# Optimization experiments

Hardware: AMD Instinct MI355X
Metric: run time of the kernel (lower is better)

Reference implementation:

```python
import jax, jax.numpy as jnp
import numpy as np

N_HEADS = 16
MAX_LEN = 1024


def setup_inputs() -> dict:
    key = jax.random.key(0)
    ks = jax.random.split(key, 6)
    B, T, C = 4, 1024, 1024
    scale = 0.02
    return {
        "x": jax.random.normal(ks[0], (B, T, C), dtype=jnp.float32),
        "qkv_w": jax.random.normal(ks[1], (3 * C, C), dtype=jnp.float32) * scale,
        "qkv_b": jax.random.normal(ks[2], (3 * C,), dtype=jnp.float32) * scale,
        "proj_w": jax.random.normal(ks[3], (C, C), dtype=jnp.float32) * scale,
        "proj_b": jax.random.normal(ks[4], (C,), dtype=jnp.float32) * scale,
        "rel_pos_emb": jax.random.normal(ks[5], (2 * MAX_LEN - 1, C), dtype=jnp.float32) * scale,
    }


def reference(x, qkv_w, qkv_b, proj_w, proj_b, rel_pos_emb):
    B, T, C = x.shape
    H = N_HEADS
    D = C // H
    # QKV projection: (B,T,3C) -> (3,B,H,T,D)
    qkv = (x @ qkv_w.T + qkv_b).reshape(B, T, 3, H, D)
    qkv = jnp.transpose(qkv, (2, 0, 3, 1, 4))
    q, k, v = qkv[0], qkv[1], qkv[2]
    # scores: (B,H,T,T)
    att = jnp.einsum("bhtd,bhsd->bhts", q, k) / np.sqrt(D).astype(np.float32)
    # Relative position bias: gather-then-sum == sum-then-gather over head_dim.
    # Pre-reduce table to (2*max_len-1, H) to avoid materializing (T,T,C).
    table = rel_pos_emb.reshape(2 * MAX_LEN - 1, H, D).sum(axis=-1)  # (2L-1, H)
    pos = jnp.arange(T)
    rel_idx = pos[:, None] - pos[None, :] + (MAX_LEN - 1)  # (T,T)
    bias = jnp.transpose(table[rel_idx], (2, 0, 1))  # (H,T,T)
    att = att + bias[None]
    # causal mask: positions j > i masked to -inf
    causal = pos[None, :] > pos[:, None]  # (T,T) True above diagonal
    att = jnp.where(causal[None, None], -jnp.inf, att)
    att = jax.nn.softmax(att, axis=-1)
    out = jnp.einsum("bhts,bhsd->bhtd", att, v)  # (B,H,T,D)
    out = jnp.transpose(out, (0, 2, 1, 3)).reshape(B, T, C)
    return out @ proj_w.T + proj_b
```

## Files before the change

### kernel.cpp

```cpp
#include <hip/hip_runtime.h>
#include <hip/hip_bf16.h>


typedef __bf16 bf16x8 __attribute__((ext_vector_type(8)));
typedef float f32x4 __attribute__((ext_vector_type(4)));

__device__ __forceinline__ float bf2f(unsigned short u) {
    return __uint_as_float(((unsigned)u) << 16);
}
__device__ __forceinline__ unsigned short f2bf(float f) {
    __hip_bfloat16 h = __float2bfloat16(f);
    return *reinterpret_cast<unsigned short*>(&h);
}
__device__ __forceinline__ int4 cvt8(float4 a, float4 b) {
    union { unsigned short s[8]; int4 v; } u;
    u.s[0] = f2bf(a.x); u.s[1] = f2bf(a.y); u.s[2] = f2bf(a.z); u.s[3] = f2bf(a.w);
    u.s[4] = f2bf(b.x); u.s[5] = f2bf(b.y); u.s[6] = f2bf(b.z); u.s[7] = f2bf(b.w);
    return u.v;
}

__global__ __launch_bounds__(256) void table_reduce(const float* __restrict__ rel,
                                                    float* __restrict__ table) {
    const int p = blockIdx.x;
    const int tid = threadIdx.x, lane = tid & 63, wave = tid >> 6;
    const float* r = rel + (size_t)p * 1024;
    float s[4];
#pragma unroll
    for (int k = 0; k < 4; ++k) s[k] = r[tid + 256 * k];
#pragma unroll
    for (int k = 0; k < 4; ++k) {
        float v = s[k];
        for (int o = 32; o; o >>= 1) v += __shfl_xor(v, o, 64);
        if (lane == 0) table[p * 16 + wave + 4 * k] = v;
    }
}

template <int EPI, bool AF32>
__global__ __launch_bounds__(512) void gemm_bt(const void* __restrict__ Ain,
                                               const float* __restrict__ Bf,
                                               const float* __restrict__ bias,
                                               unsigned short* __restrict__ outb,
                                               float* __restrict__ outf,
                                               int M, int N, int K) {
    __shared__ __attribute__((aligned(16))) unsigned short As[128 * 40];
    __shared__ __attribute__((aligned(16))) unsigned short Bs[128 * 40];
    const int bm = blockIdx.x * 128, bn = blockIdx.y * 128;
    const int tid = threadIdx.x, lane = tid & 63, wave = tid >> 6;
    const int wr = wave & 1, wc = wave >> 1;
    const int quad = lane >> 4, lm = lane & 15;

    const int srow = tid >> 2;
    const int scol = (tid & 3) * 8;
    const float* ApF          = (const float*)Ain + (size_t)(bm + srow) * K + scol;
    const unsigned short* ApH = (const unsigned short*)Ain + (size_t)(bm + srow) * K + scol;
    const float* BpF          = Bf + (size_t)(bn + srow) * K + scol;
    unsigned short* AsW = &As[srow * 40 + scol];
    unsigned short* BsW = &Bs[srow * 40 + scol];

    f32x4 acc[4][2];
#pragma unroll
    for (int r = 0; r < 4; ++r)
#pragma unroll
        for (int c = 0; c < 2; ++c) acc[r][c] = (f32x4){0.f, 0.f, 0.f, 0.f};

    float4 paf0, paf1, pbf0, pbf1;
    int4 pah;
    if (AF32) {
        paf0 = *(const float4*)(ApF);
        paf1 = *(const float4*)(ApF + 4);
    } else {
        pah = *(const int4*)(ApH);
    }
    pbf0 = *(const float4*)(BpF);
    pbf1 = *(const float4*)(BpF + 4);

    for (int kk = 0; kk < K; kk += 32) {
        *(int4*)(AsW) = AF32 ? cvt8(paf0, paf1) : pah;
        *(int4*)(BsW) = cvt8(pbf0, pbf1);
        __syncthreads();

        if (kk + 32 < K) {
            if (AF32) {
                paf0 = *(const float4*)(ApF + kk + 32);
                paf1 = *(const float4*)(ApF + kk + 36);
            } else {
                pah = *(const int4*)(ApH + kk + 32);
            }
            pbf0 = *(const float4*)(BpF + kk + 32);
            pbf1 = *(const float4*)(BpF + kk + 36);
        }

        bf16x8 af[4], bfr[2];
#pragma unroll
        for (int r = 0; r < 4; ++r)
            af[r] = *(const bf16x8*)(&As[(64 * wr + 16 * r + lm) * 40 + quad * 8]);
#pragma unroll
        for (int c = 0; c < 2; ++c)
            bfr[c] = *(const bf16x8*)(&Bs[(32 * wc + 16 * c + lm) * 40 + quad * 8]);
#pragma unroll
        for (int r = 0; r < 4; ++r)
#pragma unroll
            for (int c = 0; c < 2; ++c)
                acc[r][c] = __builtin_amdgcn_mfma_f32_16x16x32_bf16(af[r], bfr[c], acc[r][c], 0, 0, 0);
        __syncthreads();
    }

#pragma unroll
    for (int r = 0; r < 4; ++r)
#pragma unroll
        for (int c = 0; c < 2; ++c)
#pragma unroll
            for (int i = 0; i < 4; ++i) {
                const int row = bm + 64 * wr + 16 * r + quad * 4 + i;
                const int col = bn + 32 * wc + 16 * c + lm;
                const float v = acc[r][c][i] + bias[col];
                if (EPI == 0) {
                    const int b = row >> 10, t = row & 1023;
                    const int s3 = col >> 10, rem = col & 1023;
                    const int h = rem >> 6, d = rem & 63;
                    const size_t base = (((size_t)s3 * 4 + b) * 16 + h) * 65536;
                    const size_t off = base + (s3 == 2 ? (size_t)d * 1024 + t
                                                       : (size_t)t * 64 + d);
                    outb[off] = f2bf(v);
                } else {
                    outf[(size_t)row * N + col] = v;
                }
            }
}

__global__ __launch_bounds__(512) void attn_mfma(const unsigned short* __restrict__ qkvb,
                                                 const float* __restrict__ table,
                                                 unsigned short* __restrict__ y) {
    const int bh = blockIdx.x, b = bh >> 4, h = bh & 15;
    const int qb = (7 - blockIdx.y) * 128;
    const int tid = threadIdx.x, lane = tid & 63, wave = tid >> 6;
    const int quad = lane >> 4, lm = lane & 15;

    __shared__ __attribute__((aligned(16))) unsigned short Ks[64][72];
    __shared__ __attribute__((aligned(16))) unsigned short Vs[64][72];
    __shared__ __attribute__((aligned(16))) unsigned short Ps[8][16][72];
    __shared__ float tb[1280];

    const unsigned short* Qg  = qkvb + ((size_t)(b)*16 + h) * 65536;
    const unsigned short* Kg  = qkvb + ((size_t)(4 + b)*16 + h) * 65536;
    const unsigned short* Vtg = qkvb + ((size_t)(8 + b)*16 + h) * 65536;

    const bf16x8 qf0 = *(const bf16x8*)(Qg + (size_t)(qb + wave * 16 + lm) * 64 + quad * 8);
    const bf16x8 qf1 = *(const bf16x8*)(Qg + (size_t)(qb + wave * 16 + lm) * 64 + 32 + quad * 8);

    const int tbn = qb + 255;
    for (int i = tid; i < tbn; i += 512) tb[i] = table[(896 + i) * 16 + h];

    f32x4 oacc[4];
#pragma unroll
    for (int nb = 0; nb < 4; ++nb) oacc[nb] = (f32x4){0.f, 0.f, 0.f, 0.f};
    float mi[4], li[4];
#pragma unroll
    for (int i = 0; i < 4; ++i) { mi[i] = -1e30f; li[i] = 0.f; }

    const int ktiles = qb / 64 + 2;
    for (int kt = 0; kt < ktiles; ++kt) {
        __syncthreads();
        {
            const int r0 = tid >> 3, c0 = (tid & 7) * 8;
            *(int4*)&Ks[r0][c0] = *(const int4*)(Kg + (size_t)(kt * 64 + r0) * 64 + c0);
            *(int4*)&Vs[r0][c0] = *(const int4*)(Vtg + (size_t)r0 * 1024 + kt * 64 + c0);
        }
        __syncthreads();

        f32x4 s[4];
#pragma unroll
        for (int nb = 0; nb < 4; ++nb) {
            bf16x8 k0 = *(const bf16x8*)(&Ks[nb * 16 + lm][quad * 8]);
            bf16x8 k1 = *(const bf16x8*)(&Ks[nb * 16 + lm][32 + quad * 8]);
            s[nb] = (f32x4){0.f, 0.f, 0.f, 0.f};
            s[nb] = __builtin_amdgcn_mfma_f32_16x16x32_bf16(qf0, k0, s[nb], 0, 0, 0);
            s[nb] = __builtin_amdgcn_mfma_f32_16x16x32_bf16(qf1, k1, s[nb], 0, 0, 0);
        }

        const int qrow0 = qb + wave * 16 + quad * 4;
        const int jbase = kt * 64 + lm;
#pragma unroll
        for (int nb = 0; nb < 4; ++nb)
#pragma unroll
            for (int i = 0; i < 4; ++i) {
                const int q = qrow0 + i, j = jbase + nb * 16;
                const float v = fmaf(s[nb][i], 0.125f, tb[q - j + 127]);
                s[nb][i] = (j <= q) ? v : -1e30f;
            }

        float mnew[4], al[4];
#pragma unroll
        for (int i = 0; i < 4; ++i) {
            float mx = fmaxf(fmaxf(s[0][i], s[1][i]), fmaxf(s[2][i], s[3][i]));
            mx = fmaxf(mx, __shfl_xor(mx, 1, 64));
            mx = fmaxf(mx, __shfl_xor(mx, 2, 64));
            mx = fmaxf(mx, __shfl_xor(mx, 4, 64));
            mx = fmaxf(mx, __shfl_xor(mx, 8, 64));
            mnew[i] = fmaxf(mi[i], mx);
            al[i] = __expf(mi[i] - mnew[i]);
            mi[i] = mnew[i];
        }
#pragma unroll
        for (int nb = 0; nb < 4; ++nb)
#pragma unroll
            for (int i = 0; i < 4; ++i) s[nb][i] = __expf(s[nb][i] - mnew[i]);
#pragma unroll
        for (int i = 0; i < 4; ++i) {
            float sm = (s[0][i] + s[1][i]) + (s[2][i] + s[3][i]);
            sm += __shfl_xor(sm, 1, 64);
            sm += __shfl_xor(sm, 2, 64);
            sm += __shfl_xor(sm, 4, 64);
            sm += __shfl_xor(sm, 8, 64);
            li[i] = li[i] * al[i] + sm;
        }

#pragma unroll
        for (int nb = 0; nb < 4; ++nb)
#pragma unroll
            for (int i = 0; i < 4; ++i)
                Ps[wave][quad * 4 + i][nb * 16 + lm] = f2bf(s[nb][i]);

#pragma unroll
        for (int nb = 0; nb < 4; ++nb)
#pragma unroll
            for (int i = 0; i < 4; ++i) oacc[nb][i] *= al[i];

        const bf16x8 p0 = *(const bf16x8*)(&Ps[wave][lm][quad * 8]);
        const bf16x8 p1 = *(const bf16x8*)(&Ps[wave][lm][32 + quad * 8]);
#pragma unroll
        for (int nb = 0; nb < 4; ++nb) {
            bf16x8 v0 = *(const bf16x8*)(&Vs[nb * 16 + lm][quad * 8]);
            bf16x8 v1 = *(const bf16x8*)(&Vs[nb * 16 + lm][32 + quad * 8]);
            oacc[nb] = __builtin_amdgcn_mfma_f32_16x16x32_bf16(p0, v0, oacc[nb], 0, 0, 0);
            oacc[nb] = __builtin_amdgcn_mfma_f32_16x16x32_bf16(p1, v1, oacc[nb], 0, 0, 0);
        }
    }

    float inv[4];
#pragma unroll
    for (int i = 0; i < 4; ++i) inv[i] = 1.0f / li[i];
#pragma unroll
    for (int nb = 0; nb < 4; ++nb)
#pragma unroll
        for (int i = 0; i < 4; ++i) {
            const int q = qb + wave * 16 + quad * 4 + i;
            const int d = nb * 16 + lm;
            y[((size_t)(b * 1024 + q)) * 1024 + h * 64 + d] = f2bf(oacc[nb][i] * inv[i]);
        }
}

extern "C" void kernel_launch(void* const* d_in, const int* in_sizes, int n_in,
                              void* d_out, int out_size, void* d_ws, size_t ws_size,
                              hipStream_t stream) {
    const float* x      = (const float*)d_in[0];
    const float* qkv_w  = (const float*)d_in[1];
    const float* qkv_b  = (const float*)d_in[2];
    const float* proj_w = (const float*)d_in[3];
    const float* proj_b = (const float*)d_in[4];
    const float* rel    = (const float*)d_in[5];
    float* out = (float*)d_out;

    char* ws = (char*)d_ws;
    float* table         = (float*)(ws + 16777216);
    unsigned short* qkvb = (unsigned short*)(ws + 16908288);
    unsigned short* yb   = (unsigned short*)(ws + 42074112);

    table_reduce<<<2047, 256, 0, stream>>>(rel, table);
    gemm_bt<0, true><<<dim3(32, 24), 512, 0, stream>>>(x, qkv_w, qkv_b, qkvb, nullptr,
                                                       4096, 3072, 1024);
    attn_mfma<<<dim3(64, 8), 512, 0, stream>>>(qkvb, table, yb);
    gemm_bt<1, false><<<dim3(32, 8), 512, 0, stream>>>(yb, proj_w, proj_b, nullptr, out,
                                                       4096, 1024, 1024);
}
```

Baseline: 205.6 us.

## Deepen GEMM K-tile to 64 and prefetch K/V tiles in attention loop

The GEMM kernel now stages 64-wide K slices in shared memory (padded row stride 72) and runs two MFMA sub-steps per barrier pair, which halves the number of loop iterations and synchronizations. The attention kernel now register-prefetches the next K/V tile while computing on the current one, so global loads overlap with compute, with the trailing barrier moved to the end of the loop. This costs more registers and shared memory per block, which may lower occupancy.

```diff
diff --git a/kernel.cpp b/kernel.cpp
--- a/kernel.cpp
+++ b/kernel.cpp
@@ -42,20 +42,20 @@
                                                unsigned short* __restrict__ outb,
                                                float* __restrict__ outf,
                                                int M, int N, int K) {
-    __shared__ __attribute__((aligned(16))) unsigned short As[128 * 40];
-    __shared__ __attribute__((aligned(16))) unsigned short Bs[128 * 40];
+    __shared__ __attribute__((aligned(16))) unsigned short As[128 * 72];
+    __shared__ __attribute__((aligned(16))) unsigned short Bs[128 * 72];
     const int bm = blockIdx.x * 128, bn = blockIdx.y * 128;
     const int tid = threadIdx.x, lane = tid & 63, wave = tid >> 6;
     const int wr = wave & 1, wc = wave >> 1;
     const int quad = lane >> 4, lm = lane & 15;
 
     const int srow = tid >> 2;
-    const int scol = (tid & 3) * 8;
+    const int scol = (tid & 3) * 16;
     const float* ApF          = (const float*)Ain + (size_t)(bm + srow) * K + scol;
     const unsigned short* ApH = (const unsigned short*)Ain + (size_t)(bm + srow) * K + scol;
     const float* BpF          = Bf + (size_t)(bn + srow) * K + scol;
-    unsigned short* AsW = &As[srow * 40 + scol];
-    unsigned short* BsW = &Bs[srow * 40 + scol];
+    unsigned short* AsW = &As[srow * 72 + scol];
+    unsigned short* BsW = &Bs[srow * 72 + scol];
 
     f32x4 acc[4][2];
 #pragma unroll
@@ -63,45 +63,60 @@
 #pragma unroll
         for (int c = 0; c < 2; ++c) acc[r][c] = (f32x4){0.f, 0.f, 0.f, 0.f};
 
-    float4 paf0, paf1, pbf0, pbf1;
-    int4 pah;
+    float4 pa0, pa1, pa2, pa3, pb0, pb1, pb2, pb3;
+    int4 pah0, pah1;
     if (AF32) {
-        paf0 = *(const float4*)(ApF);
-        paf1 = *(const float4*)(ApF + 4);
+        pa0 = *(const float4*)(ApF);
+        pa1 = *(const float4*)(ApF + 4);
+        pa2 = *(const float4*)(ApF + 8);
+        pa3 = *(const float4*)(ApF + 12);
     } else {
-        pah = *(const int4*)(ApH);
-    }
-    pbf0 = *(const float4*)(BpF);
-    pbf1 = *(const float4*)(BpF + 4);
-
-    for (int kk = 0; kk < K; kk += 32) {
-        *(int4*)(AsW) = AF32 ? cvt8(paf0, paf1) : pah;
-        *(int4*)(BsW) = cvt8(pbf0, pbf1);
-        __syncthreads();
-
-        if (kk + 32 < K) {
+        pah0 = *(const int4*)(ApH);
+        pah1 = *(const int4*)(ApH + 8);
+    }
+    pb0 = *(const float4*)(BpF);
+    pb1 = *(const float4*)(BpF + 4);
+    pb2 = *(const float4*)(BpF + 8);
+    pb3 = *(const float4*)(BpF + 12);
+
+    for (int kk = 0; kk < K; kk += 64) {
+        *(int4*)(AsW)     = AF32 ? cvt8(pa0, pa1) : pah0;
+        *(int4*)(AsW + 8) = AF32 ? cvt8(pa2, pa3) : pah1;
+        *(int4*)(BsW)     = cvt8(pb0, pb1);
+        *(int4*)(BsW + 8) = cvt8(pb2, pb3);
+        __syncthreads();
+
+        if (kk + 64 < K) {
             if (AF32) {
-                paf0 = *(const float4*)(ApF + kk + 32);
-                paf1 = *(const float4*)(ApF + kk + 36);
+                pa0 = *(const float4*)(ApF + kk + 64);
+                pa1 = *(const float4*)(ApF + kk + 68);
+                pa2 = *(const float4*)(ApF + kk + 72);
+                pa3 = *(const float4*)(ApF + kk + 76);
             } else {
-                pah = *(const int4*)(ApH + kk + 32);
+                pah0 = *(const int4*)(ApH + kk + 64);
+                pah1 = *(const int4*)(ApH + kk + 72);
             }
-            pbf0 = *(const float4*)(BpF + kk + 32);
-            pbf1 = *(const float4*)(BpF + kk + 36);
-        }
-
-        bf16x8 af[4], bfr[2];
-#pragma unroll
-        for (int r = 0; r < 4; ++r)
-            af[r] = *(const bf16x8*)(&As[(64 * wr + 16 * r + lm) * 40 + quad * 8]);
-#pragma unroll
-        for (int c = 0; c < 2; ++c)
-            bfr[c] = *(const bf16x8*)(&Bs[(32 * wc + 16 * c + lm) * 40 + quad * 8]);
-#pragma unroll
-        for (int r = 0; r < 4; ++r)
+            pb0 = *(const float4*)(BpF + kk + 64);
+            pb1 = *(const float4*)(BpF + kk + 68);
+            pb2 = *(const float4*)(BpF + kk + 72);
+            pb3 = *(const float4*)(BpF + kk + 76);
+        }
+
+#pragma unroll
+        for (int ks = 0; ks < 2; ++ks) {
+            bf16x8 af[4], bfr[2];
+#pragma unroll
+            for (int r = 0; r < 4; ++r)
+                af[r] = *(const bf16x8*)(&As[(64 * wr + 16 * r + lm) * 72 + ks * 32 + quad * 8]);
 #pragma unroll
             for (int c = 0; c < 2; ++c)
-                acc[r][c] = __builtin_amdgcn_mfma_f32_16x16x32_bf16(af[r], bfr[c], acc[r][c], 0, 0, 0);
+                bfr[c] = *(const bf16x8*)(&Bs[(32 * wc + 16 * c + lm) * 72 + ks * 32 + quad * 8]);
+#pragma unroll
+            for (int r = 0; r < 4; ++r)
+#pragma unroll
+                for (int c = 0; c < 2; ++c)
+                    acc[r][c] = __builtin_amdgcn_mfma_f32_16x16x32_bf16(af[r], bfr[c], acc[r][c], 0, 0, 0);
+        }
         __syncthreads();
     }
 
@@ -158,15 +173,19 @@
 #pragma unroll
     for (int i = 0; i < 4; ++i) { mi[i] = -1e30f; li[i] = 0.f; }
 
+    const int r0 = tid >> 3, c0 = (tid & 7) * 8;
+    int4 pk = *(const int4*)(Kg + (size_t)r0 * 64 + c0);
+    int4 pv = *(const int4*)(Vtg + (size_t)r0 * 1024 + c0);
+
     const int ktiles = qb / 64 + 2;
     for (int kt = 0; kt < ktiles; ++kt) {
-        __syncthreads();
-        {
-            const int r0 = tid >> 3, c0 = (tid & 7) * 8;
-            *(int4*)&Ks[r0][c0] = *(const int4*)(Kg + (size_t)(kt * 64 + r0) * 64 + c0);
-            *(int4*)&Vs[r0][c0] = *(const int4*)(Vtg + (size_t)r0 * 1024 + kt * 64 + c0);
-        }
-        __syncthreads();
+        *(int4*)&Ks[r0][c0] = pk;
+        *(int4*)&Vs[r0][c0] = pv;
+        __syncthreads();
+        if (kt + 1 < ktiles) {
+            pk = *(const int4*)(Kg + (size_t)((kt + 1) * 64 + r0) * 64 + c0);
+            pv = *(const int4*)(Vtg + (size_t)r0 * 1024 + (kt + 1) * 64 + c0);
+        }
 
         f32x4 s[4];
 #pragma unroll
@@ -235,6 +254,7 @@
             oacc[nb] = __builtin_amdgcn_mfma_f32_16x16x32_bf16(p0, v0, oacc[nb], 0, 0, 0);
             oacc[nb] = __builtin_amdgcn_mfma_f32_16x16x32_bf16(p1, v1, oacc[nb], 0, 0, 0);
         }
+        __syncthreads();
     }
 
     float inv[4];
```

Result: slower. 217.9 us (+6.0%).

## Prefetch K/V tiles into registers and transpose S MFMA for per-lane softmax rows

Applied to the files above, without the earlier changes.

The attention loop now loads the next K and V tiles from global memory into registers while the current tile is being computed, which hides global load latency behind the MFMA work. It also swaps the operand order of the QK^T MFMA so each lane holds one query row across its accumulators. The row max and sum then need only two cross-lane shuffles instead of four shuffles per row for four rows, and the P tile is written to LDS with packed 8-byte stores. The cost is extra shuffles to broadcast alpha and 1/l back into the output layout, plus more live registers for the prefetch buffers.

```diff
diff --git a/kernel.cpp b/kernel.cpp
--- a/kernel.cpp
+++ b/kernel.cpp
@@ -154,19 +154,22 @@
     f32x4 oacc[4];
 #pragma unroll
     for (int nb = 0; nb < 4; ++nb) oacc[nb] = (f32x4){0.f, 0.f, 0.f, 0.f};
-    float mi[4], li[4];
-#pragma unroll
-    for (int i = 0; i < 4; ++i) { mi[i] = -1e30f; li[i] = 0.f; }
-
+    float mi = -1e30f, li = 0.f;
+
+    const int r0 = tid >> 3, c0 = (tid & 7) * 8;
+    int4 pk = *(const int4*)(Kg + (size_t)r0 * 64 + c0);
+    int4 pv = *(const int4*)(Vtg + (size_t)r0 * 1024 + c0);
+
+    const int q = qb + wave * 16 + lm;
     const int ktiles = qb / 64 + 2;
     for (int kt = 0; kt < ktiles; ++kt) {
-        __syncthreads();
-        {
-            const int r0 = tid >> 3, c0 = (tid & 7) * 8;
-            *(int4*)&Ks[r0][c0] = *(const int4*)(Kg + (size_t)(kt * 64 + r0) * 64 + c0);
-            *(int4*)&Vs[r0][c0] = *(const int4*)(Vtg + (size_t)r0 * 1024 + kt * 64 + c0);
-        }
-        __syncthreads();
+        *(int4*)&Ks[r0][c0] = pk;
+        *(int4*)&Vs[r0][c0] = pv;
+        __syncthreads();
+        if (kt + 1 < ktiles) {
+            pk = *(const int4*)(Kg + (size_t)((kt + 1) * 64 + r0) * 64 + c0);
+            pv = *(const int4*)(Vtg + (size_t)r0 * 1024 + (kt + 1) * 64 + c0);
+        }
 
         f32x4 s[4];
 #pragma unroll
@@ -174,57 +177,59 @@
             bf16x8 k0 = *(const bf16x8*)(&Ks[nb * 16 + lm][quad * 8]);
             bf16x8 k1 = *(const bf16x8*)(&Ks[nb * 16 + lm][32 + quad * 8]);
             s[nb] = (f32x4){0.f, 0.f, 0.f, 0.f};
-            s[nb] = __builtin_amdgcn_mfma_f32_16x16x32_bf16(qf0, k0, s[nb], 0, 0, 0);
-            s[nb] = __builtin_amdgcn_mfma_f32_16x16x32_bf16(qf1, k1, s[nb], 0, 0, 0);
-        }
-
-        const int qrow0 = qb + wave * 16 + quad * 4;
-        const int jbase = kt * 64 + lm;
+            s[nb] = __builtin_amdgcn_mfma_f32_16x16x32_bf16(k0, qf0, s[nb], 0, 0, 0);
+            s[nb] = __builtin_amdgcn_mfma_f32_16x16x32_bf16(k1, qf1, s[nb], 0, 0, 0);
+        }
+
+        const int jb0 = kt * 64 + quad * 4;
 #pragma unroll
         for (int nb = 0; nb < 4; ++nb)
 #pragma unroll
             for (int i = 0; i < 4; ++i) {
-                const int q = qrow0 + i, j = jbase + nb * 16;
+                const int j = jb0 + nb * 16 + i;
                 const float v = fmaf(s[nb][i], 0.125f, tb[q - j + 127]);
                 s[nb][i] = (j <= q) ? v : -1e30f;
             }
 
-        float mnew[4], al[4];
-#pragma unroll
-        for (int i = 0; i < 4; ++i) {
-            float mx = fmaxf(fmaxf(s[0][i], s[1][i]), fmaxf(s[2][i], s[3][i]));
-            mx = fmaxf(mx, __shfl_xor(mx, 1, 64));
-            mx = fmaxf(mx, __shfl_xor(mx, 2, 64));
-            mx = fmaxf(mx, __shfl_xor(mx, 4, 64));
-            mx = fmaxf(mx, __shfl_xor(mx, 8, 64));
-            mnew[i] = fmaxf(mi[i], mx);
-            al[i] = __expf(mi[i] - mnew[i]);
-            mi[i] = mnew[i];
-        }
-#pragma unroll
-        for (int nb = 0; nb < 4; ++nb)
-#pragma unroll
-            for (int i = 0; i < 4; ++i) s[nb][i] = __expf(s[nb][i] - mnew[i]);
-#pragma unroll
-        for (int i = 0; i < 4; ++i) {
-            float sm = (s[0][i] + s[1][i]) + (s[2][i] + s[3][i]);
-            sm += __shfl_xor(sm, 1, 64);
-            sm += __shfl_xor(sm, 2, 64);
-            sm += __shfl_xor(sm, 4, 64);
-            sm += __shfl_xor(sm, 8, 64);
-            li[i] = li[i] * al[i] + sm;
-        }
-
-#pragma unroll
-        for (int nb = 0; nb < 4; ++nb)
-#pragma unroll
-            for (int i = 0; i < 4; ++i)
-                Ps[wave][quad * 4 + i][nb * 16 + lm] = f2bf(s[nb][i]);
-
-#pragma unroll
-        for (int nb = 0; nb < 4; ++nb)
-#pragma unroll
-            for (int i = 0; i < 4; ++i) oacc[nb][i] *= al[i];
+        float mx = -1e30f;
+#pragma unroll
+        for (int nb = 0; nb < 4; ++nb)
+#pragma unroll
+            for (int i = 0; i < 4; ++i) mx = fmaxf(mx, s[nb][i]);
+        mx = fmaxf(mx, __shfl_xor(mx, 16, 64));
+        mx = fmaxf(mx, __shfl_xor(mx, 32, 64));
+        const float mnew = fmaxf(mi, mx);
+        const float alpha = __expf(mi - mnew);
+        mi = mnew;
+#pragma unroll
+        for (int nb = 0; nb < 4; ++nb)
+#pragma unroll
+            for (int i = 0; i < 4; ++i) s[nb][i] = __expf(s[nb][i] - mnew);
+        float ps = 0.f;
+#pragma unroll
+        for (int nb = 0; nb < 4; ++nb)
+            ps += (s[nb][0] + s[nb][1]) + (s[nb][2] + s[nb][3]);
+        ps += __shfl_xor(ps, 16, 64);
+        ps += __shfl_xor(ps, 32, 64);
+        li = li * alpha + ps;
+
+#pragma unroll
+        for (int nb = 0; nb < 4; ++nb) {
+            union { unsigned short u[4]; int2 v; } p4;
+            p4.u[0] = f2bf(s[nb][0]);
+            p4.u[1] = f2bf(s[nb][1]);
+            p4.u[2] = f2bf(s[nb][2]);
+            p4.u[3] = f2bf(s[nb][3]);
+            *(int2*)(&Ps[wave][lm][nb * 16 + quad * 4]) = p4.v;
+        }
+
+        float alr[4];
+#pragma unroll
+        for (int i = 0; i < 4; ++i) alr[i] = __shfl(alpha, quad * 4 + i, 64);
+#pragma unroll
+        for (int nb = 0; nb < 4; ++nb)
+#pragma unroll
+            for (int i = 0; i < 4; ++i) oacc[nb][i] *= alr[i];
 
         const bf16x8 p0 = *(const bf16x8*)(&Ps[wave][lm][quad * 8]);
         const bf16x8 p1 = *(const bf16x8*)(&Ps[wave][lm][32 + quad * 8]);
@@ -235,18 +240,20 @@
             oacc[nb] = __builtin_amdgcn_mfma_f32_16x16x32_bf16(p0, v0, oacc[nb], 0, 0, 0);
             oacc[nb] = __builtin_amdgcn_mfma_f32_16x16x32_bf16(p1, v1, oacc[nb], 0, 0, 0);
         }
-    }
-
-    float inv[4];
-#pragma unroll
-    for (int i = 0; i < 4; ++i) inv[i] = 1.0f / li[i];
+        __syncthreads();
+    }
+
+    const float linv = 1.0f / li;
+    float invr[4];
+#pragma unroll
+    for (int i = 0; i < 4; ++i) invr[i] = __shfl(linv, quad * 4 + i, 64);
 #pragma unroll
     for (int nb = 0; nb < 4; ++nb)
 #pragma unroll
         for (int i = 0; i < 4; ++i) {
-            const int q = qb + wave * 16 + quad * 4 + i;
+            const int qq = qb + wave * 16 + quad * 4 + i;
             const int d = nb * 16 + lm;
-            y[((size_t)(b * 1024 + q)) * 1024 + h * 64 + d] = f2bf(oacc[nb][i] * inv[i]);
+            y[((size_t)(b * 1024 + qq)) * 1024 + h * 64 + d] = f2bf(oacc[nb][i] * invr[i]);
         }
 }
 
```

Result: faster. 193.1 us (-6.1%).
